# Kernel optimization log

Measured on AMD Instinct MI355X. Metric: run time of the kernel, lower is better.

The kernel has to match this reference:

```python
import jax, jax.numpy as jnp
import numpy as np

B, C, H, W = 32, 256, 56, 56   # batch, in_channels, spatial
OC, R, K = 256, 64, 3          # out_channels, low rank, kernel size
PAD, STRIDE = 1, 1


def setup_inputs() -> dict:
    key = jax.random.key(0)
    kx, ku, kv = jax.random.split(key, 3)
    x = jax.random.normal(kx, (B, C, H, W), dtype=jnp.float32)
    # Per-offset low-rank factors: U[i,j] is (out_c, r), V[i,j] is (r, in_c),
    # matching nn.ParameterDict of 1x1 conv weights in the torch module.
    U = jax.random.normal(ku, (K, K, OC, R), dtype=jnp.float32) * 0.05
    V = jax.random.normal(kv, (K, K, R, C), dtype=jnp.float32) * 0.05
    return {"x": x, "U": U, "V": V}


def reference(x, U, V):
    k = U.shape[0]
    pad, stride = PAD, STRIDE
    b, c, h_in, w_in = x.shape
    h_out = (h_in + 2 * pad - (k - 1) - 1) // stride + 1
    w_out = (w_in + 2 * pad - (k - 1) - 1) // stride + 1
    xp = jnp.pad(x, ((0, 0), (0, 0), (pad, pad), (pad, pad)))
    total = jnp.zeros((b, U.shape[2], h_out, w_out), dtype=x.dtype)
    # Loop over the k*k fixed spatial offsets (structurally distinct params),
    # using strided views instead of materializing the unfolded tensor.
    for i in range(k):
        for j in range(k):
            sl = xp[:, :, i:i + (h_out - 1) * stride + 1:stride,
                          j:j + (w_out - 1) * stride + 1:stride]  # [b,c,ho,wo]
            t = jnp.einsum('bchw,rc->brhw', sl, V[i, j])          # V 1x1 conv
            total = total + jnp.einsum('brhw,or->bohw', t, U[i, j])  # U 1x1 conv
    return total
```

## Files before the change

kernel.cpp:

```cpp
#include <hip/hip_runtime.h>
#include <hip/hip_bf16.h>
#include <stdint.h>
#include <stddef.h>

typedef __hip_bfloat16 bf16;
typedef __attribute__((ext_vector_type(8))) short bf16x8;
typedef __attribute__((ext_vector_type(4))) float f32x4;

namespace {
constexpr int kB = 32, kC = 256, kH = 56, kW = 56, kOC = 256, kR = 64;
constexpr int kHP = 58, kWP = 58;
constexpr int kPlane = kH * kW;
constexpr int kNPix  = kB * kPlane;
constexpr int kBM = 128, kBN = 128, kBK = 32;
constexpr int kKSteps = 9 * (kC / kBK);
}

__device__ __forceinline__ void gload16(const void* g, void* lds_wave_uniform) {
    __builtin_amdgcn_global_load_lds(
        (const __attribute__((address_space(1))) uint32_t*)(uintptr_t)g,
        (__attribute__((address_space(3))) uint32_t*)(uint32_t)(uintptr_t)lds_wave_uniform,
        16, 0, 0);
}

__global__ void merge_weights(const float* __restrict__ U, const float* __restrict__ V,
                              bf16* __restrict__ Wb) {
    const int tap = blockIdx.x >> 8;
    const int o   = blockIdx.x & 255;
    const int c   = threadIdx.x;
    const float* u = U + (size_t)(tap * kOC + o) * kR;
    const float* v = V + (size_t)(tap * kR) * kC + c;
    float acc = 0.f;
#pragma unroll
    for (int r = 0; r < kR; ++r) acc += u[r] * v[r * kC];
    Wb[(size_t)(tap * kOC + o) * kC + c] = __float2bfloat16(acc);
}

__global__ void pad_nhwc(const float* __restrict__ x, bf16* __restrict__ xt) {
    const int b  = blockIdx.x / kHP;
    const int hp = blockIdx.x % kHP;
    const int c  = threadIdx.x;
    bf16* dst = xt + ((size_t)(b * kHP + hp)) * (kWP * kC) + c;
    const bf16 zero = __float2bfloat16(0.f);
    if (hp == 0 || hp == kHP - 1) {
        for (int wp = 0; wp < kWP; ++wp) dst[(size_t)wp * kC] = zero;
        return;
    }
    const int h = hp - 1;
    dst[0] = zero;
    dst[(size_t)(kWP - 1) * kC] = zero;
    const float* src = x + ((size_t)(b * kC + c) * kH + h) * kW;
    for (int w0 = 0; w0 < kW; w0 += 4) {
        const float4 v4 = *reinterpret_cast<const float4*>(src + w0);
        dst[(size_t)(w0 + 1) * kC] = __float2bfloat16(v4.x);
        dst[(size_t)(w0 + 2) * kC] = __float2bfloat16(v4.y);
        dst[(size_t)(w0 + 3) * kC] = __float2bfloat16(v4.z);
        dst[(size_t)(w0 + 4) * kC] = __float2bfloat16(v4.w);
    }
}

__global__ __launch_bounds__(256, 2)
void conv_mfma(const bf16* __restrict__ Wb, const bf16* __restrict__ xt,
               float* __restrict__ out) {
    __shared__ bf16 Asm[kBM * kBK];
    __shared__ bf16 Bsm[kBN * kBK];

    const int tid  = threadIdx.x;
    const int lane = tid & 63;
    const int wid  = tid >> 6;
    const int p0   = blockIdx.x * kBN;
    const int ocb  = blockIdx.y * kBM;

    const int row1 = wid * 32 + (lane >> 2);
    const int row2 = row1 + 16;
    const int coff = (lane & 3) * 8;

    const bf16* gA1 = Wb + (size_t)(ocb + row1) * kC + coff;
    const bf16* gA2 = Wb + (size_t)(ocb + row2) * kC + coff;

    const int gp1 = p0 + row1;
    const int gp2 = p0 + row2;
    const int b1 = gp1 / kPlane, q1 = gp1 - b1 * kPlane;
    const int b2 = gp2 / kPlane, q2 = gp2 - b2 * kPlane;
    const int h1 = q1 / kW, w1 = q1 - h1 * kW;
    const int h2 = q2 / kW, w2 = q2 - h2 * kW;
    const bf16* gB1 = xt + ((size_t)((b1 * kHP + h1) * kWP + w1)) * kC + coff;
    const bf16* gB2 = xt + ((size_t)((b2 * kHP + h2) * kWP + w2)) * kC + coff;

    char* AsmB = (char*)Asm + wid * 2048;
    char* BsmB = (char*)Bsm + wid * 2048;

    const int wr = wid >> 1, wc = wid & 1;
    const int lrow = lane & 15;
    const int lk   = (lane >> 4) * 8;

    f32x4 acc[4][4] = {};

    for (int ks = 0; ks < kKSteps; ++ks) {
        const int tap  = ks >> 3;
        const int c0   = (ks & 7) * kBK;
        const int aoff = tap * (kOC * kC) + c0;
        const int boff = ((tap / 3) * kWP + (tap % 3)) * kC + c0;

        gload16(gA1 + aoff, AsmB);
        gload16(gA2 + aoff, AsmB + 1024);
        gload16(gB1 + boff, BsmB);
        gload16(gB2 + boff, BsmB + 1024);
        __syncthreads();

        bf16x8 af[4], bfr[4];
#pragma unroll
        for (int mi = 0; mi < 4; ++mi)
            af[mi] = *(const bf16x8*)&Asm[(wr * 64 + mi * 16 + lrow) * kBK + lk];
#pragma unroll
        for (int nj = 0; nj < 4; ++nj)
            bfr[nj] = *(const bf16x8*)&Bsm[(wc * 64 + nj * 16 + lrow) * kBK + lk];
#pragma unroll
        for (int mi = 0; mi < 4; ++mi)
#pragma unroll
            for (int nj = 0; nj < 4; ++nj)
                acc[mi][nj] = __builtin_amdgcn_mfma_f32_16x16x32_bf16(
                    af[mi], bfr[nj], acc[mi][nj], 0, 0, 0);
        __syncthreads();
    }

#pragma unroll
    for (int nj = 0; nj < 4; ++nj) {
        const int gp = p0 + wc * 64 + nj * 16 + lrow;
        const int bb = gp / kPlane;
        const int qq = gp - bb * kPlane;
        float* ob = out + (size_t)bb * (kOC * kPlane) + qq;
#pragma unroll
        for (int mi = 0; mi < 4; ++mi) {
            const int o = ocb + wr * 64 + mi * 16 + (lane >> 4) * 4;
            float* op = ob + (size_t)o * kPlane;
#pragma unroll
            for (int r = 0; r < 4; ++r)
                op[(size_t)r * kPlane] = acc[mi][nj][r];
        }
    }
}

extern "C" void kernel_launch(void* const* d_in, const int* in_sizes, int n_in,
                              void* d_out, int out_size, void* d_ws, size_t ws_size,
                              hipStream_t stream) {
    const float* x = (const float*)d_in[0];
    const float* U = (const float*)d_in[1];
    const float* V = (const float*)d_in[2];
    float* out = (float*)d_out;

    bf16* Wb = (bf16*)d_ws;
    bf16* xt = (bf16*)((char*)d_ws + (size_t)9 * kOC * kC * 2);

    merge_weights<<<dim3(9 * kOC), dim3(kC), 0, stream>>>(U, V, Wb);
    pad_nhwc<<<dim3(kB * kHP), dim3(kC), 0, stream>>>(x, xt);
    conv_mfma<<<dim3(kNPix / kBN, kOC / kBM), dim3(256), 0, stream>>>(Wb, xt, out);
}
```

Before: 362.0 us.

## Double-buffer conv LDS tiles, swizzle LDS/blocks, and transpose pad via shared memory

The conv kernel now double-buffers its A/B LDS tiles so the next K-step's global-to-LDS loads overlap the current MFMA work, with one wait+barrier per step instead of two. It also XOR-swizzles LDS column offsets to cut bank conflicts, remaps block IDs across 8 groups to improve L2 locality, and raises launch bounds to 4 blocks per SM. The pad/transpose kernel stages a row through shared memory, so global reads are coalesced float4 loads and writes are packed dword stores. The costs are more LDS per block and a hand-written waitcnt/barrier whose correctness depends on the async-load semantics.

New measurement: 344.1 us. -5.0%, faster.

```diff
diff --git a/kernel.cpp b/kernel.cpp
--- a/kernel.cpp
+++ b/kernel.cpp
@@ -21,6 +21,12 @@
         (const __attribute__((address_space(1))) uint32_t*)(uintptr_t)g,
         (__attribute__((address_space(3))) uint32_t*)(uint32_t)(uintptr_t)lds_wave_uniform,
         16, 0, 0);
+}
+
+__device__ __forceinline__ unsigned short f2bf(float f) {
+    union { float f; unsigned int u; } cv; cv.f = f;
+    const unsigned int u = cv.u;
+    return (unsigned short)((u + 0x7FFFu + ((u >> 16) & 1u)) >> 16);
 }
 
 __global__ void merge_weights(const float* __restrict__ U, const float* __restrict__ V,
@@ -36,50 +42,79 @@
     Wb[(size_t)(tap * kOC + o) * kC + c] = __float2bfloat16(acc);
 }
 
-__global__ void pad_nhwc(const float* __restrict__ x, bf16* __restrict__ xt) {
+__global__ __launch_bounds__(256)
+void pad_nhwc(const float* __restrict__ x, bf16* __restrict__ xt) {
     const int b  = blockIdx.x / kHP;
     const int hp = blockIdx.x % kHP;
-    const int c  = threadIdx.x;
-    bf16* dst = xt + ((size_t)(b * kHP + hp)) * (kWP * kC) + c;
-    const bf16 zero = __float2bfloat16(0.f);
+    const int tid = threadIdx.x;
+    bf16* dst = xt + (size_t)(b * kHP + hp) * (kWP * kC);
+
     if (hp == 0 || hp == kHP - 1) {
-        for (int wp = 0; wp < kWP; ++wp) dst[(size_t)wp * kC] = zero;
+        uint4* d4 = (uint4*)dst;
+        constexpr int n16 = (kWP * kC * 2) / 16;
+        for (int i = tid; i < n16; i += 256) d4[i] = uint4{0, 0, 0, 0};
         return;
     }
+
     const int h = hp - 1;
-    dst[0] = zero;
-    dst[(size_t)(kWP - 1) * kC] = zero;
-    const float* src = x + ((size_t)(b * kC + c) * kH + h) * kW;
-    for (int w0 = 0; w0 < kW; w0 += 4) {
-        const float4 v4 = *reinterpret_cast<const float4*>(src + w0);
-        dst[(size_t)(w0 + 1) * kC] = __float2bfloat16(v4.x);
-        dst[(size_t)(w0 + 2) * kC] = __float2bfloat16(v4.y);
-        dst[(size_t)(w0 + 3) * kC] = __float2bfloat16(v4.z);
-        dst[(size_t)(w0 + 4) * kC] = __float2bfloat16(v4.w);
-    }
-}
-
-__global__ __launch_bounds__(256, 2)
+    __shared__ unsigned short t[256][58];
+
+    const int w4 = tid & 15;
+    const int cb = tid >> 4;
+#pragma unroll
+    for (int pass = 0; pass < 16; ++pass) {
+        const int c = pass * 16 + cb;
+        if (w4 < 14) {
+            const float4 v = *reinterpret_cast<const float4*>(
+                x + ((size_t)(b * kC + c) * kH + h) * kW + w4 * 4);
+            t[c][w4 * 4 + 0] = f2bf(v.x);
+            t[c][w4 * 4 + 1] = f2bf(v.y);
+            t[c][w4 * 4 + 2] = f2bf(v.z);
+            t[c][w4 * 4 + 3] = f2bf(v.w);
+        }
+    }
+    __syncthreads();
+
+    const int c2   = (tid & 127) * 2;
+    const int half = tid >> 7;
+    unsigned int* dw = (unsigned int*)dst;
+#pragma unroll
+    for (int wpi = 0; wpi < 29; ++wpi) {
+        const int wp = wpi * 2 + half;
+        unsigned int val = 0;
+        if (wp >= 1 && wp <= kW) {
+            const int w = wp - 1;
+            val = (unsigned int)t[c2][w] | ((unsigned int)t[c2 + 1][w] << 16);
+        }
+        dw[(size_t)wp * 128 + (c2 >> 1)] = val;
+    }
+}
+
+__global__ __launch_bounds__(256, 4)
 void conv_mfma(const bf16* __restrict__ Wb, const bf16* __restrict__ xt,
                float* __restrict__ out) {
-    __shared__ bf16 Asm[kBM * kBK];
-    __shared__ bf16 Bsm[kBN * kBK];
+    __shared__ bf16 Asm[2][kBM * kBK];
+    __shared__ bf16 Bsm[2][kBM * kBK];
 
     const int tid  = threadIdx.x;
     const int lane = tid & 63;
     const int wid  = tid >> 6;
-    const int p0   = blockIdx.x * kBN;
-    const int ocb  = blockIdx.y * kBM;
-
-    const int row1 = wid * 32 + (lane >> 2);
-    const int row2 = row1 + 16;
-    const int coff = (lane & 3) * 8;
+
+    const int bid = blockIdx.x;
+    constexpr int cpx = (kNPix / kBN) * (kOC / kBM) / 8;
+    const int swz = (bid & 7) * cpx + (bid >> 3);
+    const int ocb = (swz & 1) * kBM;
+    const int p0  = (swz >> 1) * kBN;
+
+    const int rowL = lane >> 2;
+    const int row1 = wid * 32 + rowL;
+    const int sw   = (lane >> 3) & 3;
+    const int coff = (((lane & 3) ^ sw)) * 8;
 
     const bf16* gA1 = Wb + (size_t)(ocb + row1) * kC + coff;
-    const bf16* gA2 = Wb + (size_t)(ocb + row2) * kC + coff;
 
     const int gp1 = p0 + row1;
-    const int gp2 = p0 + row2;
+    const int gp2 = gp1 + 16;
     const int b1 = gp1 / kPlane, q1 = gp1 - b1 * kPlane;
     const int b2 = gp2 / kPlane, q2 = gp2 - b2 * kPlane;
     const int h1 = q1 / kW, w1 = q1 - h1 * kW;
@@ -87,41 +122,50 @@
     const bf16* gB1 = xt + ((size_t)((b1 * kHP + h1) * kWP + w1)) * kC + coff;
     const bf16* gB2 = xt + ((size_t)((b2 * kHP + h2) * kWP + w2)) * kC + coff;
 
-    char* AsmB = (char*)Asm + wid * 2048;
-    char* BsmB = (char*)Bsm + wid * 2048;
-
     const int wr = wid >> 1, wc = wid & 1;
     const int lrow = lane & 15;
-    const int lk   = (lane >> 4) * 8;
+    const int rcs  = (((lane >> 4) ^ ((lrow >> 1) & 3))) * 8;
 
     f32x4 acc[4][4] = {};
 
-    for (int ks = 0; ks < kKSteps; ++ks) {
+    auto stage = [&](int buf, int ks) {
         const int tap  = ks >> 3;
         const int c0   = (ks & 7) * kBK;
         const int aoff = tap * (kOC * kC) + c0;
         const int boff = ((tap / 3) * kWP + (tap % 3)) * kC + c0;
-
-        gload16(gA1 + aoff, AsmB);
-        gload16(gA2 + aoff, AsmB + 1024);
-        gload16(gB1 + boff, BsmB);
-        gload16(gB2 + boff, BsmB + 1024);
-        __syncthreads();
-
+        char* AsmB = (char*)(&Asm[buf][0]) + wid * 2048;
+        char* BsmB = (char*)(&Bsm[buf][0]) + wid * 2048;
+        gload16(gA1 + aoff,           AsmB);
+        gload16(gA1 + aoff + 16 * kC, AsmB + 1024);
+        gload16(gB1 + boff,           BsmB);
+        gload16(gB2 + boff,           BsmB + 1024);
+    };
+
+    stage(0, 0);
+    asm volatile("s_waitcnt vmcnt(0)\ns_barrier" ::: "memory");
+
+    int cur = 0;
+    for (int ks = 0; ks < kKSteps; ++ks) {
+        if (ks + 1 < kKSteps) stage(cur ^ 1, ks + 1);
+
+        const bf16* Acur = &Asm[cur][0];
+        const bf16* Bcur = &Bsm[cur][0];
         bf16x8 af[4], bfr[4];
 #pragma unroll
         for (int mi = 0; mi < 4; ++mi)
-            af[mi] = *(const bf16x8*)&Asm[(wr * 64 + mi * 16 + lrow) * kBK + lk];
+            af[mi] = *(const bf16x8*)&Acur[(wr * 64 + mi * 16 + lrow) * kBK + rcs];
 #pragma unroll
         for (int nj = 0; nj < 4; ++nj)
-            bfr[nj] = *(const bf16x8*)&Bsm[(wc * 64 + nj * 16 + lrow) * kBK + lk];
+            bfr[nj] = *(const bf16x8*)&Bcur[(wc * 64 + nj * 16 + lrow) * kBK + rcs];
 #pragma unroll
         for (int mi = 0; mi < 4; ++mi)
 #pragma unroll
             for (int nj = 0; nj < 4; ++nj)
                 acc[mi][nj] = __builtin_amdgcn_mfma_f32_16x16x32_bf16(
                     af[mi], bfr[nj], acc[mi][nj], 0, 0, 0);
-        __syncthreads();
+
+        asm volatile("s_waitcnt vmcnt(0)\ns_barrier" ::: "memory");
+        cur ^= 1;
     }
 
 #pragma unroll
@@ -153,6 +197,6 @@
     bf16* xt = (bf16*)((char*)d_ws + (size_t)9 * kOC * kC * 2);
 
     merge_weights<<<dim3(9 * kOC), dim3(kC), 0, stream>>>(U, V, Wb);
-    pad_nhwc<<<dim3(kB * kHP), dim3(kC), 0, stream>>>(x, xt);
-    conv_mfma<<<dim3(kNPix / kBN, kOC / kBM), dim3(256), 0, stream>>>(Wb, xt, out);
-}
+    pad_nhwc<<<dim3(kB * kHP), dim3(256), 0, stream>>>(x, xt);
+    conv_mfma<<<dim3(kNPix / kBN * (kOC / kBM)), dim3(256), 0, stream>>>(Wb, xt, out);
+}
```
